# Optimization experiments

Measured on AMD Instinct MI355X. Metric: run time of the kernel, lower is better.

Reference implementation:

```python
import jax, jax.numpy as jnp
import numpy as np

B, T = 64, 512
OBS_DIM, USER_DIM = 512, 128
HID, MLP_HID = 512, 512
E, R, K = 8, 8, 3
TAU = 2.0


def setup_inputs() -> dict:
    key = jax.random.key(0)
    ks = jax.random.split(key, 32)
    f32 = jnp.float32

    def rn(k, shape, scale=1.0):
        return jax.random.normal(k, shape, dtype=f32) * scale

    inp = {
        'user_emb': rn(ks[0], (B, USER_DIM)),
        'obs': rn(ks[1], (B, T, OBS_DIM)),
        # gating MLP: Linear(user_dim,128) -> ReLU -> Linear(128,E)
        'gw1': rn(ks[2], (USER_DIM, 128), 1 / np.sqrt(USER_DIM)),
        'gb1': jnp.zeros((128,), f32),
        'gw2': rn(ks[3], (128, E), 1 / np.sqrt(128)),
        'gb2': jnp.zeros((E,), f32),
        # obs_proj MoLELinear(obs_dim, hidden)
        'op_w': rn(ks[4], (OBS_DIM, HID), 1 / np.sqrt(OBS_DIM)),
        'op_b': jnp.zeros((HID,), f32),
        'op_As': rn(ks[5], (OBS_DIM, R), 1 / np.sqrt(OBS_DIM)),
        'op_Bs': rn(ks[6], (R, HID), 0.02),
        'op_Ae': rn(ks[7], (E, OBS_DIM, R), 1 / np.sqrt(OBS_DIM)),
        'op_Be': rn(ks[8], (E, R, HID), 0.02),
        # two Conv1d(hidden, hidden, k=3, pad=1) layers, OIH layout
        'cw1': rn(ks[9], (HID, HID, K), 1 / np.sqrt(HID * K)),
        'cb1': jnp.zeros((HID,), f32),
        'cw2': rn(ks[10], (HID, HID, K), 1 / np.sqrt(HID * K)),
        'cb2': jnp.zeros((HID,), f32),
        # head_1 MoLELinear(hidden, mlp_hidden)
        'h1_w': rn(ks[11], (HID, MLP_HID), 1 / np.sqrt(HID)),
        'h1_b': jnp.zeros((MLP_HID,), f32),
        'h1_As': rn(ks[12], (HID, R), 1 / np.sqrt(HID)),
        'h1_Bs': rn(ks[13], (R, MLP_HID), 0.02),
        'h1_Ae': rn(ks[14], (E, HID, R), 1 / np.sqrt(HID)),
        'h1_Be': rn(ks[15], (E, R, MLP_HID), 0.02),
        # head_2 MoLELinear(mlp_hidden, 1)
        'h2_w': rn(ks[16], (MLP_HID, 1), 1 / np.sqrt(MLP_HID)),
        'h2_b': jnp.zeros((1,), f32),
        'h2_As': rn(ks[17], (MLP_HID, R), 1 / np.sqrt(MLP_HID)),
        'h2_Bs': rn(ks[18], (R, 1), 0.02),
        'h2_Ae': rn(ks[19], (E, MLP_HID, R), 1 / np.sqrt(MLP_HID)),
        'h2_Be': rn(ks[20], (E, R, 1), 0.02),
    }
    return inp


def _mole(x, w, b, As, Bs, Ae, Be, rw):
    # base linear + shared LoRA + routed per-expert LoRA (dense sum of E low-rank paths)
    base = x @ w + b
    shared = (x @ As) @ Bs
    if x.ndim == 3:  # [B,T,in]
        t = jnp.einsum('bti,eir->bter', x, Ae)           # low-rank projection per expert
        expert = jnp.einsum('be,bter,ero->bto', rw, t, Be)
    else:  # [B,in]
        t = jnp.einsum('bi,eir->ber', x, Ae)
        expert = jnp.einsum('be,ber,ero->bo', rw, t, Be)
    return base + shared + expert


def _conv1d(x, w, bias):
    # x: [B,C,T], w: [O,I,K], 'same' padding (K//2)
    y = jax.lax.conv_general_dilated(x, w, window_strides=(1,), padding='SAME',
                                     dimension_numbers=('NCH', 'OIH', 'NCH'))
    return y + bias[None, :, None]


def reference(user_emb, obs, gw1, gb1, gw2, gb2,
              op_w, op_b, op_As, op_Bs, op_Ae, op_Be,
              cw1, cb1, cw2, cb2,
              h1_w, h1_b, h1_As, h1_Bs, h1_Ae, h1_Be,
              h2_w, h2_b, h2_As, h2_Bs, h2_Ae, h2_Be):
    # gating -> straight-through hard top-1 routing (training-mode path)
    z = jax.nn.relu(user_emb @ gw1 + gb1) @ gw2 + gb2
    soft = jax.nn.softmax(z / TAU, axis=-1)
    hard = jax.nn.one_hot(jnp.argmax(soft, axis=-1), soft.shape[-1], dtype=soft.dtype)
    rw = hard - jax.lax.stop_gradient(soft) + soft

    h = jax.nn.leaky_relu(_mole(obs, op_w, op_b, op_As, op_Bs, op_Ae, op_Be, rw))  # [B,T,H]
    x = jnp.transpose(h, (0, 2, 1))                      # [B,H,T]
    x = jax.nn.leaky_relu(_conv1d(x, cw1, cb1))
    x = jax.nn.leaky_relu(_conv1d(x, cw2, cb2))
    x = jnp.max(x, axis=2)                               # max_pool1d over full T -> [B,H]
    x = jax.nn.leaky_relu(_mole(x, h1_w, h1_b, h1_As, h1_Bs, h1_Ae, h1_Be, rw))
    out = _mole(x, h2_w, h2_b, h2_As, h2_Bs, h2_Ae, h2_Be, rw)[:, 0]  # [B]
    return out
```

## Files before the change

kernel.cpp:

```cpp
#include <hip/hip_runtime.h>
#include <cstdint>

typedef _Float16 f16;
typedef _Float16 f16x8 __attribute__((ext_vector_type(8)));
typedef _Float16 f16x4 __attribute__((ext_vector_type(4)));
typedef float f32x4 __attribute__((ext_vector_type(4)));

#define NB   64
#define NT   512
#define NH   512
#define NE   8
#define NR   8
#define PADT 514

__device__ __forceinline__ void load_lds16(const void* g, void* l) {
  __builtin_amdgcn_global_load_lds(
      (const __attribute__((address_space(1))) uint32_t*)g,
      (__attribute__((address_space(3))) uint32_t*)l, 16, 0, 0);
}

__device__ __forceinline__ void atomicMaxF(float* a, float v) {
  if (v >= 0.f) atomicMax((int*)a, __float_as_int(v));
  else          atomicMin((unsigned int*)a, __float_as_uint(v));
}

__global__ void gating_kernel(const float* __restrict__ ue, const float* __restrict__ gw1,
                              const float* __restrict__ gb1, const float* __restrict__ gw2,
                              const float* __restrict__ gb2, int* __restrict__ eidx) {
  const int b = blockIdx.x;
  __shared__ float ues[128];
  __shared__ float g1[128];
  __shared__ float zs[NE];
  const int j = threadIdx.x;
  ues[j] = ue[b * 128 + j];
  __syncthreads();
  float acc = gb1[j];
  for (int k = 0; k < 128; ++k) acc += ues[k] * gw1[k * 128 + j];
  g1[j] = fmaxf(acc, 0.f);
  __syncthreads();
  if (j < NE) {
    float z = gb2[j];
    for (int k = 0; k < 128; ++k) z += g1[k] * gw2[k * NE + j];
    zs[j] = z;
  }
  __syncthreads();
  if (j == 0) {
    int best = 0; float bz = zs[0];
    for (int e = 1; e < NE; ++e) if (zs[e] > bz) { bz = zs[e]; best = e; }
    eidx[b] = best;
  }
}

template <typename OT>
__global__ void fold_mole(const float* __restrict__ w, const float* __restrict__ As,
                          const float* __restrict__ Bs, const float* __restrict__ Ae,
                          const float* __restrict__ Be, OT* __restrict__ out) {
  const int i = blockIdx.x;
  const int e = blockIdx.y;
  const int k = threadIdx.x;
  float acc = w[(long)k * NH + i];
#pragma unroll
  for (int r = 0; r < NR; ++r) acc += As[k * NR + r] * Bs[r * NH + i];
  const float* Aep = Ae + ((long)e * NH + k) * NR;
  const float* Bep = Be + (long)e * NR * NH + i;
#pragma unroll
  for (int r = 0; r < NR; ++r) acc += Aep[r] * Bep[(long)r * NH];
  out[((long)e * NH + i) * NH + k] = (OT)acc;
}

__global__ void fold_h2(const float* __restrict__ w, const float* __restrict__ As,
                        const float* __restrict__ Bs, const float* __restrict__ Ae,
                        const float* __restrict__ Be, float* __restrict__ out) {
  const int e = blockIdx.x, k = threadIdx.x;
  float acc = w[k];
#pragma unroll
  for (int r = 0; r < NR; ++r) acc += As[k * NR + r] * Bs[r];
#pragma unroll
  for (int r = 0; r < NR; ++r) acc += Ae[((long)e * NH + k) * NR + r] * Be[e * NR + r];
  out[e * NH + k] = acc;
}

__global__ void pack_conv(const float* __restrict__ cw, f16* __restrict__ wp) {
  const int o = blockIdx.x, i = threadIdx.x;
  const float* s = cw + ((long)o * NH + i) * 3;
#pragma unroll
  for (int dt = 0; dt < 3; ++dt)
    wp[((long)dt * NH + o) * NH + i] = (f16)s[dt];
}

__global__ void cvt_obs(const float* __restrict__ in, f16* __restrict__ outp) {
  const int r = blockIdx.x;
  const int b = r >> 9, t = r & 511;
  const int c = threadIdx.x * 4;
  const float4 v = *(const float4*)(in + (long)r * NH + c);
  f16x4 o; o[0] = (f16)v.x; o[1] = (f16)v.y; o[2] = (f16)v.z; o[3] = (f16)v.w;
  *(f16x4*)(outp + ((long)b * PADT + 1 + t) * NH + c) = o;
}

__global__ void zero_pads(f16* __restrict__ h, f16* __restrict__ y, float* __restrict__ pooled) {
  const int b = blockIdx.x, t = threadIdx.x;
  const long s = (long)b * PADT * NH;
  h[s + t] = (f16)0; h[s + (long)513 * NH + t] = (f16)0;
  y[s + t] = (f16)0; y[s + (long)513 * NH + t] = (f16)0;
  pooled[b * NH + t] = -__builtin_inff();
}

template <int NACC, bool PSB, bool POOL>
__global__ __launch_bounds__(256, 2) void gemm_nt(
    const f16* __restrict__ A, long sA, int shiftA,
    const f16* __restrict__ Bm, long sBe, long sBacc,
    const float* __restrict__ bias,
    f16* __restrict__ O, long sO, int oRowOff,
    float* __restrict__ pooledOut,
    const int* __restrict__ eidx) {
  constexpr int BM = 128, BN = 128, BK = 64, LDK = 512;
  __shared__ __align__(16) f16 As[BM * BK];
  __shared__ __align__(16) f16 Bs[BN * BK];
  const int b = blockIdx.z;
  const int mt = blockIdx.x, nt = blockIdx.y;
  const int tid = threadIdx.x;
  const int wid = tid >> 6, lane = tid & 63;
  const int wm = wid >> 1, wn = wid & 1;
  const f16* Abase = A + (long)b * sA + (long)mt * BM * LDK;
  const f16* Bbase = Bm + (PSB ? (long)eidx[b] * sBe : 0) + (long)nt * BN * LDK;

  f32x4 acc[4][4] = {};

  const int srow = tid >> 3;
  const int sc = tid & 7;

  for (int a = 0; a < NACC; ++a) {
    const f16* Aa = Abase + (long)a * shiftA;
    const f16* Ba = Bbase + (long)a * sBacc;
    for (int kt = 0; kt < LDK / BK; ++kt) {
      __syncthreads();
#pragma unroll
      for (int i = 0; i < 4; ++i) {
        const int row = i * 32 + srow;
        const int cs = sc ^ (row & 7);
        load_lds16(Aa + (long)row * LDK + kt * BK + cs * 8,
                   (char*)As + i * 4096 + wid * 1024);
        load_lds16(Ba + (long)row * LDK + kt * BK + cs * 8,
                   (char*)Bs + i * 4096 + wid * 1024);
      }
      __syncthreads();
#pragma unroll
      for (int kk = 0; kk < BK / 32; ++kk) {
        f16x8 af[4], bf[4];
#pragma unroll
        for (int mi = 0; mi < 4; ++mi) {
          const int row = wm * 64 + mi * 16 + (lane & 15);
          const int cc = (kk * 4 + (lane >> 4)) ^ (row & 7);
          af[mi] = *(const f16x8*)(As + row * BK + cc * 8);
        }
#pragma unroll
        for (int ni = 0; ni < 4; ++ni) {
          const int row = wn * 64 + ni * 16 + (lane & 15);
          const int cc = (kk * 4 + (lane >> 4)) ^ (row & 7);
          bf[ni] = *(const f16x8*)(Bs + row * BK + cc * 8);
        }
#pragma unroll
        for (int mi = 0; mi < 4; ++mi)
#pragma unroll
          for (int ni = 0; ni < 4; ++ni)
            acc[mi][ni] = __builtin_amdgcn_mfma_f32_16x16x32_f16(af[mi], bf[ni], acc[mi][ni], 0, 0, 0);
      }
    }
  }

  const int c0 = lane & 15, r0 = (lane >> 4) * 4;
  if (POOL) {
#pragma unroll
    for (int ni = 0; ni < 4; ++ni) {
      const int gcol = nt * BN + wn * 64 + ni * 16 + c0;
      const float bv = bias[gcol];
      float m = -3.0e38f;
#pragma unroll
      for (int mi = 0; mi < 4; ++mi)
#pragma unroll
        for (int r = 0; r < 4; ++r) {
          float v = acc[mi][ni][r] + bv;
          v = v > 0.f ? v : 0.01f * v;
          m = fmaxf(m, v);
        }
      m = fmaxf(m, __shfl_xor(m, 16, 64));
      m = fmaxf(m, __shfl_xor(m, 32, 64));
      if ((lane >> 4) == 0) atomicMaxF(pooledOut + (long)b * NH + gcol, m);
    }
  } else {
#pragma unroll
    for (int ni = 0; ni < 4; ++ni) {
      const int gcol = nt * BN + wn * 64 + ni * 16 + c0;
      const float bv = bias[gcol];
#pragma unroll
      for (int mi = 0; mi < 4; ++mi) {
        const int grow = mt * BM + wm * 64 + mi * 16 + r0;
        f16* op = O + (long)b * sO + (long)(grow + oRowOff) * NH + gcol;
#pragma unroll
        for (int r = 0; r < 4; ++r) {
          float v = acc[mi][ni][r] + bv;
          v = v > 0.f ? v : 0.01f * v;
          op[(long)r * NH] = (f16)v;
        }
      }
    }
  }
}

__global__ void head1_kernel(const float* __restrict__ pooled, const float* __restrict__ W,
                             const float* __restrict__ bias, const int* __restrict__ eidx,
                             float* __restrict__ x1) {
  const int b = blockIdx.x, oc = blockIdx.y;
  const int tid = threadIdx.x;
  const int ol = tid & 127;
  const int o  = oc * 128 + ol;
  const int ks = tid >> 7;
  __shared__ float xs[NH];
  __shared__ float red[4][128];
  xs[tid] = pooled[b * NH + tid];
  __syncthreads();
  const float* wrow = W + ((long)eidx[b] * NH + o) * NH + ks * 128;
  const float* xp = xs + ks * 128;
  float acc = 0.f;
#pragma unroll 8
  for (int k = 0; k < 128; k += 4) {
    const float4 w4 = *(const float4*)(wrow + k);
    acc += xp[k] * w4.x + xp[k + 1] * w4.y + xp[k + 2] * w4.z + xp[k + 3] * w4.w;
  }
  red[ks][ol] = acc;
  __syncthreads();
  if (tid < 128) {
    const int oo = oc * 128 + tid;
    float v = red[0][tid] + red[1][tid] + red[2][tid] + red[3][tid] + bias[oo];
    x1[b * NH + oo] = v > 0.f ? v : 0.01f * v;
  }
}

__global__ void head2_kernel(const float* __restrict__ x1, const float* __restrict__ w2f,
                             const float* __restrict__ b2, const int* __restrict__ eidx,
                             float* __restrict__ out) {
  const int b = blockIdx.x, t = threadIdx.x;
  const float* w = w2f + (long)eidx[b] * NH;
  const float* x = x1 + (long)b * NH;
  float acc = 0.f;
  for (int k = t; k < NH; k += 256) acc += x[k] * w[k];
  __shared__ float red[4];
  for (int off = 32; off; off >>= 1) acc += __shfl_down(acc, off, 64);
  if ((t & 63) == 0) red[t >> 6] = acc;
  __syncthreads();
  if (t == 0) out[b] = red[0] + red[1] + red[2] + red[3] + b2[0];
}

extern "C" void kernel_launch(void* const* d_in, const int* in_sizes, int n_in,
                              void* d_out, int out_size, void* d_ws, size_t ws_size,
                              hipStream_t stream) {
  const float* user_emb = (const float*)d_in[0];
  const float* obs   = (const float*)d_in[1];
  const float* gw1   = (const float*)d_in[2];
  const float* gb1   = (const float*)d_in[3];
  const float* gw2   = (const float*)d_in[4];
  const float* gb2   = (const float*)d_in[5];
  const float* op_w  = (const float*)d_in[6];
  const float* op_b  = (const float*)d_in[7];
  const float* op_As = (const float*)d_in[8];
  const float* op_Bs = (const float*)d_in[9];
  const float* op_Ae = (const float*)d_in[10];
  const float* op_Be = (const float*)d_in[11];
  const float* cw1   = (const float*)d_in[12];
  const float* cb1   = (const float*)d_in[13];
  const float* cw2   = (const float*)d_in[14];
  const float* cb2   = (const float*)d_in[15];
  const float* h1_w  = (const float*)d_in[16];
  const float* h1_b  = (const float*)d_in[17];
  const float* h1_As = (const float*)d_in[18];
  const float* h1_Bs = (const float*)d_in[19];
  const float* h1_Ae = (const float*)d_in[20];
  const float* h1_Be = (const float*)d_in[21];
  const float* h2_w  = (const float*)d_in[22];
  const float* h2_b  = (const float*)d_in[23];
  const float* h2_As = (const float*)d_in[24];
  const float* h2_Bs = (const float*)d_in[25];
  const float* h2_Ae = (const float*)d_in[26];
  const float* h2_Be = (const float*)d_in[27];
  float* out = (float*)d_out;

  char* ws = (char*)d_ws;
  size_t off = 0;
  auto carve = [&](size_t bytes) -> void* {
    void* p = ws + off;
    off += (bytes + 255) & ~(size_t)255;
    return p;
  };
  int*   eidx   = (int*)carve(NB * sizeof(int));
  f16*   WeT    = (f16*)carve((size_t)NE * NH * NH * sizeof(f16));
  float* W1T    = (float*)carve((size_t)NE * NH * NH * sizeof(float));
  float* w2f    = (float*)carve((size_t)NE * NH * sizeof(float));
  f16*   w1p    = (f16*)carve((size_t)3 * NH * NH * sizeof(f16));
  f16*   w2p    = (f16*)carve((size_t)3 * NH * NH * sizeof(f16));
  float* pooled = (float*)carve((size_t)NB * NH * sizeof(float));
  float* x1     = (float*)carve((size_t)NB * NH * sizeof(float));
  f16*   hbuf   = (f16*)carve((size_t)NB * PADT * NH * sizeof(f16));
  f16*   ybuf   = (f16*)carve((size_t)NB * PADT * NH * sizeof(f16));
  f16*   obs_h  = ybuf + NH;
  (void)ws_size; (void)in_sizes; (void)n_in; (void)out_size;

  gating_kernel<<<NB, 128, 0, stream>>>(user_emb, gw1, gb1, gw2, gb2, eidx);
  fold_mole<f16><<<dim3(NH, NE), NH, 0, stream>>>(op_w, op_As, op_Bs, op_Ae, op_Be, WeT);
  fold_mole<float><<<dim3(NH, NE), NH, 0, stream>>>(h1_w, h1_As, h1_Bs, h1_Ae, h1_Be, W1T);
  fold_h2<<<NE, NH, 0, stream>>>(h2_w, h2_As, h2_Bs, h2_Ae, h2_Be, w2f);
  pack_conv<<<NH, NH, 0, stream>>>(cw1, w1p);
  pack_conv<<<NH, NH, 0, stream>>>(cw2, w2p);
  cvt_obs<<<NB * NT, 128, 0, stream>>>(obs, ybuf);
  zero_pads<<<NB, NH, 0, stream>>>(hbuf, ybuf, pooled);

  dim3 gg(4, 4, NB);
  gemm_nt<1, true, false><<<gg, 256, 0, stream>>>(obs_h, (long)PADT * NH, 0,
                                                  WeT, (long)NH * NH, 0,
                                                  op_b, hbuf, (long)PADT * NH, 1,
                                                  nullptr, eidx);
  gemm_nt<3, false, false><<<gg, 256, 0, stream>>>(hbuf, (long)PADT * NH, NH,
                                                   w1p, 0, (long)NH * NH,
                                                   cb1, ybuf, (long)PADT * NH, 1,
                                                   nullptr, eidx);
  gemm_nt<3, false, true><<<gg, 256, 0, stream>>>(ybuf, (long)PADT * NH, NH,
                                                  w2p, 0, (long)NH * NH,
                                                  cb2, nullptr, 0, 0,
                                                  pooled, eidx);

  head1_kernel<<<dim3(NB, 4), 512, 0, stream>>>(pooled, W1T, h1_b, eidx, x1);
  head2_kernel<<<NB, 256, 0, stream>>>(x1, w2f, h2_b, eidx, out);
}
```

Before: 342.7 us.

## Fuse prep kernels, convert obs inside GEMM, reuse A tile across conv taps

Merges gating, the weight folds, the conv packing and the pad zeroing into one multi-role prep kernel to cut launch count. The first GEMM now reads fp32 obs directly and converts it to fp16 while staging into LDS, which removes the separate cvt_obs pass and its intermediate buffer. The conv GEMMs load one 130-row A tile (with a halo) per k-step and reuse it for all three taps through row offsets, instead of reloading A once per tap. The cost is more LDS for the three B tiles, a manual non-async A load in the first GEMM, and extra halo-load logic.

New measurement: 319.1 us. 1.07x faster.

```diff
diff --git a/kernel.cpp b/kernel.cpp
--- a/kernel.cpp
+++ b/kernel.cpp
@@ -3,7 +3,6 @@
 
 typedef _Float16 f16;
 typedef _Float16 f16x8 __attribute__((ext_vector_type(8)));
-typedef _Float16 f16x4 __attribute__((ext_vector_type(4)));
 typedef float f32x4 __attribute__((ext_vector_type(4)));
 
 #define NB   64
@@ -24,140 +23,178 @@
   else          atomicMin((unsigned int*)a, __float_as_uint(v));
 }
 
-__global__ void gating_kernel(const float* __restrict__ ue, const float* __restrict__ gw1,
-                              const float* __restrict__ gb1, const float* __restrict__ gw2,
-                              const float* __restrict__ gb2, int* __restrict__ eidx) {
-  const int b = blockIdx.x;
-  __shared__ float ues[128];
-  __shared__ float g1[128];
+#define PREP_BLOCKS 9352
+__global__ __launch_bounds__(512) void prep_kernel(
+    const float* __restrict__ ue, const float* __restrict__ gw1, const float* __restrict__ gb1,
+    const float* __restrict__ gw2, const float* __restrict__ gb2,
+    const float* __restrict__ op_w, const float* __restrict__ op_As, const float* __restrict__ op_Bs,
+    const float* __restrict__ op_Ae, const float* __restrict__ op_Be,
+    const float* __restrict__ h1_w, const float* __restrict__ h1_As, const float* __restrict__ h1_Bs,
+    const float* __restrict__ h1_Ae, const float* __restrict__ h1_Be,
+    const float* __restrict__ h2_w, const float* __restrict__ h2_As, const float* __restrict__ h2_Bs,
+    const float* __restrict__ h2_Ae, const float* __restrict__ h2_Be,
+    const float* __restrict__ cw1, const float* __restrict__ cw2,
+    int* __restrict__ eidx, f16* __restrict__ WeT, float* __restrict__ W1T,
+    float* __restrict__ w2f, f16* __restrict__ w1p, f16* __restrict__ w2p,
+    f16* __restrict__ hbuf, f16* __restrict__ ybuf, float* __restrict__ pooled) {
+  const int blk = blockIdx.x;
+  const int tid = threadIdx.x;
+  __shared__ float sbufA[128];
+  __shared__ float sbufB[128];
   __shared__ float zs[NE];
-  const int j = threadIdx.x;
-  ues[j] = ue[b * 128 + j];
-  __syncthreads();
-  float acc = gb1[j];
-  for (int k = 0; k < 128; ++k) acc += ues[k] * gw1[k * 128 + j];
-  g1[j] = fmaxf(acc, 0.f);
-  __syncthreads();
-  if (j < NE) {
-    float z = gb2[j];
-    for (int k = 0; k < 128; ++k) z += g1[k] * gw2[k * NE + j];
-    zs[j] = z;
-  }
-  __syncthreads();
-  if (j == 0) {
-    int best = 0; float bz = zs[0];
-    for (int e = 1; e < NE; ++e) if (zs[e] > bz) { bz = zs[e]; best = e; }
-    eidx[b] = best;
-  }
-}
-
-template <typename OT>
-__global__ void fold_mole(const float* __restrict__ w, const float* __restrict__ As,
-                          const float* __restrict__ Bs, const float* __restrict__ Ae,
-                          const float* __restrict__ Be, OT* __restrict__ out) {
-  const int i = blockIdx.x;
-  const int e = blockIdx.y;
-  const int k = threadIdx.x;
-  float acc = w[(long)k * NH + i];
-#pragma unroll
-  for (int r = 0; r < NR; ++r) acc += As[k * NR + r] * Bs[r * NH + i];
-  const float* Aep = Ae + ((long)e * NH + k) * NR;
-  const float* Bep = Be + (long)e * NR * NH + i;
-#pragma unroll
-  for (int r = 0; r < NR; ++r) acc += Aep[r] * Bep[(long)r * NH];
-  out[((long)e * NH + i) * NH + k] = (OT)acc;
-}
-
-__global__ void fold_h2(const float* __restrict__ w, const float* __restrict__ As,
-                        const float* __restrict__ Bs, const float* __restrict__ Ae,
-                        const float* __restrict__ Be, float* __restrict__ out) {
-  const int e = blockIdx.x, k = threadIdx.x;
-  float acc = w[k];
-#pragma unroll
-  for (int r = 0; r < NR; ++r) acc += As[k * NR + r] * Bs[r];
-#pragma unroll
-  for (int r = 0; r < NR; ++r) acc += Ae[((long)e * NH + k) * NR + r] * Be[e * NR + r];
-  out[e * NH + k] = acc;
-}
-
-__global__ void pack_conv(const float* __restrict__ cw, f16* __restrict__ wp) {
-  const int o = blockIdx.x, i = threadIdx.x;
-  const float* s = cw + ((long)o * NH + i) * 3;
-#pragma unroll
-  for (int dt = 0; dt < 3; ++dt)
-    wp[((long)dt * NH + o) * NH + i] = (f16)s[dt];
-}
-
-__global__ void cvt_obs(const float* __restrict__ in, f16* __restrict__ outp) {
-  const int r = blockIdx.x;
-  const int b = r >> 9, t = r & 511;
-  const int c = threadIdx.x * 4;
-  const float4 v = *(const float4*)(in + (long)r * NH + c);
-  f16x4 o; o[0] = (f16)v.x; o[1] = (f16)v.y; o[2] = (f16)v.z; o[3] = (f16)v.w;
-  *(f16x4*)(outp + ((long)b * PADT + 1 + t) * NH + c) = o;
-}
-
-__global__ void zero_pads(f16* __restrict__ h, f16* __restrict__ y, float* __restrict__ pooled) {
-  const int b = blockIdx.x, t = threadIdx.x;
-  const long s = (long)b * PADT * NH;
-  h[s + t] = (f16)0; h[s + (long)513 * NH + t] = (f16)0;
-  y[s + t] = (f16)0; y[s + (long)513 * NH + t] = (f16)0;
-  pooled[b * NH + t] = -__builtin_inff();
-}
-
-template <int NACC, bool PSB, bool POOL>
-__global__ __launch_bounds__(256, 2) void gemm_nt(
-    const f16* __restrict__ A, long sA, int shiftA,
+
+  if (blk < 64) {
+    const int b = blk;
+    if (tid < 128) sbufA[tid] = ue[b * 128 + tid];
+    __syncthreads();
+    if (tid < 128) {
+      float acc = gb1[tid];
+      for (int k = 0; k < 128; ++k) acc += sbufA[k] * gw1[k * 128 + tid];
+      sbufB[tid] = fmaxf(acc, 0.f);
+    }
+    __syncthreads();
+    if (tid < NE) {
+      float z = gb2[tid];
+      for (int k = 0; k < 128; ++k) z += sbufB[k] * gw2[k * NE + tid];
+      zs[tid] = z;
+    }
+    __syncthreads();
+    if (tid == 0) {
+      int best = 0; float bz = zs[0];
+      for (int e = 1; e < NE; ++e) if (zs[e] > bz) { bz = zs[e]; best = e; }
+      eidx[b] = best;
+    }
+  } else if (blk < 64 + 4096) {
+    const int q = blk - 64;
+    const int i = q & 511, e = q >> 9, k = tid;
+    float acc = op_w[(long)k * NH + i];
+#pragma unroll
+    for (int r = 0; r < NR; ++r) acc += op_As[k * NR + r] * op_Bs[r * NH + i];
+    const float* Aep = op_Ae + ((long)e * NH + k) * NR;
+    const float* Bep = op_Be + (long)e * NR * NH + i;
+#pragma unroll
+    for (int r = 0; r < NR; ++r) acc += Aep[r] * Bep[(long)r * NH];
+    WeT[((long)e * NH + i) * NH + k] = (f16)acc;
+  } else if (blk < 4160 + 4096) {
+    const int q = blk - 4160;
+    const int i = q & 511, e = q >> 9, k = tid;
+    float acc = h1_w[(long)k * NH + i];
+#pragma unroll
+    for (int r = 0; r < NR; ++r) acc += h1_As[k * NR + r] * h1_Bs[r * NH + i];
+    const float* Aep = h1_Ae + ((long)e * NH + k) * NR;
+    const float* Bep = h1_Be + (long)e * NR * NH + i;
+#pragma unroll
+    for (int r = 0; r < NR; ++r) acc += Aep[r] * Bep[(long)r * NH];
+    W1T[((long)e * NH + i) * NH + k] = acc;
+  } else if (blk < 8256 + 8) {
+    const int e = blk - 8256, k = tid;
+    float acc = h2_w[k];
+#pragma unroll
+    for (int r = 0; r < NR; ++r) acc += h2_As[k * NR + r] * h2_Bs[r];
+#pragma unroll
+    for (int r = 0; r < NR; ++r) acc += h2_Ae[((long)e * NH + k) * NR + r] * h2_Be[e * NR + r];
+    w2f[e * NH + k] = acc;
+  } else if (blk < 8264 + 512) {
+    const int o = blk - 8264, i = tid;
+    const float* s = cw1 + ((long)o * NH + i) * 3;
+#pragma unroll
+    for (int dt = 0; dt < 3; ++dt) w1p[((long)dt * NH + o) * NH + i] = (f16)s[dt];
+  } else if (blk < 8776 + 512) {
+    const int o = blk - 8776, i = tid;
+    const float* s = cw2 + ((long)o * NH + i) * 3;
+#pragma unroll
+    for (int dt = 0; dt < 3; ++dt) w2p[((long)dt * NH + o) * NH + i] = (f16)s[dt];
+  } else {
+    const int b = blk - 9288, t = tid;
+    const long s = (long)b * PADT * NH;
+    hbuf[s + t] = (f16)0; hbuf[s + (long)513 * NH + t] = (f16)0;
+    ybuf[s + t] = (f16)0; ybuf[s + (long)513 * NH + t] = (f16)0;
+    pooled[b * NH + t] = -__builtin_inff();
+  }
+}
+
+template <int NDT, bool F32A, bool PSB, bool POOL>
+__global__ __launch_bounds__(256, 2) void fgemm(
+    const f16* __restrict__ A, const float* __restrict__ A32, long sA,
     const f16* __restrict__ Bm, long sBe, long sBacc,
     const float* __restrict__ bias,
     f16* __restrict__ O, long sO, int oRowOff,
     float* __restrict__ pooledOut,
     const int* __restrict__ eidx) {
-  constexpr int BM = 128, BN = 128, BK = 64, LDK = 512;
-  __shared__ __align__(16) f16 As[BM * BK];
-  __shared__ __align__(16) f16 Bs[BN * BK];
+  constexpr int BK = 64, LDK = 512;
+  constexpr int ASLOTS = (NDT == 3) ? 132 : 128;
+  constexpr int SOFF = (NDT == 3) ? 1 : 0;
+  __shared__ __align__(16) f16 A_lds[ASLOTS * BK];
+  __shared__ __align__(16) f16 B_lds[NDT * 128 * BK];
   const int b = blockIdx.z;
   const int mt = blockIdx.x, nt = blockIdx.y;
   const int tid = threadIdx.x;
   const int wid = tid >> 6, lane = tid & 63;
   const int wm = wid >> 1, wn = wid & 1;
-  const f16* Abase = A + (long)b * sA + (long)mt * BM * LDK;
-  const f16* Bbase = Bm + (PSB ? (long)eidx[b] * sBe : 0) + (long)nt * BN * LDK;
+  const f16* Ab = F32A ? nullptr : (A + (long)b * sA + (long)mt * 128 * LDK);
+  const float* A32b = F32A ? (A32 + (long)b * sA + (long)mt * 128 * LDK) : nullptr;
+  const f16* Bb = Bm + (PSB ? (long)eidx[b] * sBe : 0) + (long)nt * 128 * LDK;
 
   f32x4 acc[4][4] = {};
 
-  const int srow = tid >> 3;
-  const int sc = tid & 7;
-
-  for (int a = 0; a < NACC; ++a) {
-    const f16* Aa = Abase + (long)a * shiftA;
-    const f16* Ba = Bbase + (long)a * sBacc;
-    for (int kt = 0; kt < LDK / BK; ++kt) {
-      __syncthreads();
+  for (int kt = 0; kt < LDK / BK; ++kt) {
+    __syncthreads();
+#pragma unroll
+    for (int d = 0; d < NDT; ++d)
+#pragma unroll
+      for (int j = 0; j < 4; ++j) {
+        const int row = j * 32 + (tid >> 3);
+        const int cs = (tid & 7) ^ (row & 7);
+        load_lds16(Bb + (long)d * sBacc + (long)row * LDK + kt * BK + cs * 8,
+                   (char*)B_lds + d * 16384 + j * 4096 + wid * 1024);
+      }
+    if (F32A) {
 #pragma unroll
       for (int i = 0; i < 4; ++i) {
-        const int row = i * 32 + srow;
-        const int cs = sc ^ (row & 7);
-        load_lds16(Aa + (long)row * LDK + kt * BK + cs * 8,
-                   (char*)As + i * 4096 + wid * 1024);
-        load_lds16(Ba + (long)row * LDK + kt * BK + cs * 8,
-                   (char*)Bs + i * 4096 + wid * 1024);
-      }
-      __syncthreads();
-#pragma unroll
-      for (int kk = 0; kk < BK / 32; ++kk) {
+        const int slot = i * 32 + (tid >> 3);
+        const float* s = A32b + (long)slot * LDK + kt * BK + (tid & 7) * 8;
+        const float4 v0 = *(const float4*)s;
+        const float4 v1 = *(const float4*)(s + 4);
+        f16x8 h;
+        h[0] = (f16)v0.x; h[1] = (f16)v0.y; h[2] = (f16)v0.z; h[3] = (f16)v0.w;
+        h[4] = (f16)v1.x; h[5] = (f16)v1.y; h[6] = (f16)v1.z; h[7] = (f16)v1.w;
+        *(f16x8*)((char*)A_lds + slot * 128 + (((tid & 7) ^ (slot & 7)) * 16)) = h;
+      }
+    } else {
+#pragma unroll
+      for (int i = 0; i < 4; ++i) {
+        const int slot = SOFF + i * 32 + (tid >> 3);
+        const int cs = (tid & 7) ^ (slot & 7);
+        load_lds16(Ab + (long)slot * LDK + kt * BK + cs * 8,
+                   (char*)A_lds + SOFF * 128 + i * 4096 + wid * 1024);
+      }
+      if (NDT == 3) {
+        if (tid < 16) {
+          const int hs = (tid < 8) ? 0 : 129;
+          const int c8 = tid & 7;
+          const int cs = c8 ^ (hs & 7);
+          const f16x8 h = *(const f16x8*)(Ab + (long)hs * LDK + kt * BK + cs * 8);
+          *(f16x8*)((char*)A_lds + hs * 128 + c8 * 16) = h;
+        }
+      }
+    }
+    __syncthreads();
+#pragma unroll
+    for (int kk = 0; kk < BK / 32; ++kk)
+#pragma unroll
+      for (int d = 0; d < NDT; ++d) {
         f16x8 af[4], bf[4];
 #pragma unroll
         for (int mi = 0; mi < 4; ++mi) {
-          const int row = wm * 64 + mi * 16 + (lane & 15);
-          const int cc = (kk * 4 + (lane >> 4)) ^ (row & 7);
-          af[mi] = *(const f16x8*)(As + row * BK + cc * 8);
+          const int slot = wm * 64 + mi * 16 + (lane & 15) + (NDT == 3 ? d : 0);
+          const int cc = (kk * 4 + (lane >> 4)) ^ (slot & 7);
+          af[mi] = *(const f16x8*)(A_lds + slot * BK + cc * 8);
         }
 #pragma unroll
         for (int ni = 0; ni < 4; ++ni) {
           const int row = wn * 64 + ni * 16 + (lane & 15);
           const int cc = (kk * 4 + (lane >> 4)) ^ (row & 7);
-          bf[ni] = *(const f16x8*)(Bs + row * BK + cc * 8);
+          bf[ni] = *(const f16x8*)(B_lds + d * 128 * BK + row * BK + cc * 8);
         }
 #pragma unroll
         for (int mi = 0; mi < 4; ++mi)
@@ -165,14 +202,13 @@
           for (int ni = 0; ni < 4; ++ni)
             acc[mi][ni] = __builtin_amdgcn_mfma_f32_16x16x32_f16(af[mi], bf[ni], acc[mi][ni], 0, 0, 0);
       }
-    }
   }
 
   const int c0 = lane & 15, r0 = (lane >> 4) * 4;
   if (POOL) {
 #pragma unroll
     for (int ni = 0; ni < 4; ++ni) {
-      const int gcol = nt * BN + wn * 64 + ni * 16 + c0;
+      const int gcol = nt * 128 + wn * 64 + ni * 16 + c0;
       const float bv = bias[gcol];
       float m = -3.0e38f;
 #pragma unroll
@@ -190,11 +226,11 @@
   } else {
 #pragma unroll
     for (int ni = 0; ni < 4; ++ni) {
-      const int gcol = nt * BN + wn * 64 + ni * 16 + c0;
+      const int gcol = nt * 128 + wn * 64 + ni * 16 + c0;
       const float bv = bias[gcol];
 #pragma unroll
       for (int mi = 0; mi < 4; ++mi) {
-        const int grow = mt * BM + wm * 64 + mi * 16 + r0;
+        const int grow = mt * 128 + wm * 64 + mi * 16 + r0;
         f16* op = O + (long)b * sO + (long)(grow + oRowOff) * NH + gcol;
 #pragma unroll
         for (int r = 0; r < 4; ++r) {
@@ -301,31 +337,29 @@
   float* x1     = (float*)carve((size_t)NB * NH * sizeof(float));
   f16*   hbuf   = (f16*)carve((size_t)NB * PADT * NH * sizeof(f16));
   f16*   ybuf   = (f16*)carve((size_t)NB * PADT * NH * sizeof(f16));
-  f16*   obs_h  = ybuf + NH;
   (void)ws_size; (void)in_sizes; (void)n_in; (void)out_size;
 
-  gating_kernel<<<NB, 128, 0, stream>>>(user_emb, gw1, gb1, gw2, gb2, eidx);
-  fold_mole<f16><<<dim3(NH, NE), NH, 0, stream>>>(op_w, op_As, op_Bs, op_Ae, op_Be, WeT);
-  fold_mole<float><<<dim3(NH, NE), NH, 0, stream>>>(h1_w, h1_As, h1_Bs, h1_Ae, h1_Be, W1T);
-  fold_h2<<<NE, NH, 0, stream>>>(h2_w, h2_As, h2_Bs, h2_Ae, h2_Be, w2f);
-  pack_conv<<<NH, NH, 0, stream>>>(cw1, w1p);
-  pack_conv<<<NH, NH, 0, stream>>>(cw2, w2p);
-  cvt_obs<<<NB * NT, 128, 0, stream>>>(obs, ybuf);
-  zero_pads<<<NB, NH, 0, stream>>>(hbuf, ybuf, pooled);
+  prep_kernel<<<PREP_BLOCKS, 512, 0, stream>>>(
+      user_emb, gw1, gb1, gw2, gb2,
+      op_w, op_As, op_Bs, op_Ae, op_Be,
+      h1_w, h1_As, h1_Bs, h1_Ae, h1_Be,
+      h2_w, h2_As, h2_Bs, h2_Ae, h2_Be,
+      cw1, cw2,
+      eidx, WeT, W1T, w2f, w1p, w2p, hbuf, ybuf, pooled);
 
   dim3 gg(4, 4, NB);
-  gemm_nt<1, true, false><<<gg, 256, 0, stream>>>(obs_h, (long)PADT * NH, 0,
-                                                  WeT, (long)NH * NH, 0,
-                                                  op_b, hbuf, (long)PADT * NH, 1,
-                                                  nullptr, eidx);
-  gemm_nt<3, false, false><<<gg, 256, 0, stream>>>(hbuf, (long)PADT * NH, NH,
-                                                   w1p, 0, (long)NH * NH,
-                                                   cb1, ybuf, (long)PADT * NH, 1,
-                                                   nullptr, eidx);
-  gemm_nt<3, false, true><<<gg, 256, 0, stream>>>(ybuf, (long)PADT * NH, NH,
-                                                  w2p, 0, (long)NH * NH,
-                                                  cb2, nullptr, 0, 0,
-                                                  pooled, eidx);
+  fgemm<1, true, true, false><<<gg, 256, 0, stream>>>(
+      nullptr, obs, (long)NT * NH,
+      WeT, (long)NH * NH, 0,
+      op_b, hbuf, (long)PADT * NH, 1, nullptr, eidx);
+  fgemm<3, false, false, false><<<gg, 256, 0, stream>>>(
+      hbuf, nullptr, (long)PADT * NH,
+      w1p, 0, (long)NH * NH,
+      cb1, ybuf, (long)PADT * NH, 1, nullptr, eidx);
+  fgemm<3, false, false, true><<<gg, 256, 0, stream>>>(
+      ybuf, nullptr, (long)PADT * NH,
+      w2p, 0, (long)NH * NH,
+      cb2, nullptr, 0, 0, pooled, eidx);
 
   head1_kernel<<<dim3(NB, 4), 512, 0, stream>>>(pooled, W1T, h1_b, eidx, x1);
   head2_kernel<<<NB, 256, 0, stream>>>(x1, w2f, h2_b, eidx, out);
```
